# Kernel tuning notes

Hardware: AMD Instinct MI355X
Metric: run time of the kernel (lower is better)

The kernel has to match this reference:

```python
import jax, jax.numpy as jnp
import numpy as np

B, S, SR, SN = 8, 1024, 256, 1024
D1 = 768; D2 = 512; D3 = 768; MVH = 256
H = 12; HDC = 32; HDR = 32; HD = 64
MLP_DIM = 3072
LN_EPS = 1e-6

def _ln(x, w):
    mu = jnp.mean(x, axis=-1, keepdims=True)
    var = jnp.var(x, axis=-1, keepdims=True)
    return (x - mu) * jax.lax.rsqrt(var + LN_EPS) * w

def _rope(x, freqs):
    # x: [B,H,S,dr]; freqs: [S, dr//2] (learned RoPE param)
    emb = jnp.concatenate([freqs, freqs], axis=-1)
    cos = jnp.cos(emb); sin = jnp.sin(emb)
    d = x.shape[-1] // 2
    rot = jnp.concatenate([-x[..., d:], x[..., :d]], axis=-1)
    return x * cos + rot * sin

def _rope_freqs(seq, dim, theta=10.0):
    inv_freq = 1.0 / theta ** (np.arange(0, dim, 2, dtype=np.float32) / dim)
    t = np.arange(seq, dtype=np.float32)
    return jnp.asarray(np.outer(t, inv_freq))

def setup_inputs():
    key = jax.random.key(0)
    ks = iter(jax.random.split(key, 48))
    n = lambda shape, s=0.02: jax.random.normal(next(ks), shape, jnp.float32) * s
    return dict(
        input_q=jax.random.normal(next(ks), (B, S, D1), jnp.float32),
        ln_q_w=jnp.ones((D1,), jnp.float32), ln_kv_w=jnp.ones((D1,), jnp.float32),
        Wt_mq=n((SR, S)), Wt_vq=n((SR, S)), Wt_mkv=n((SR, S)), Wt_vkv=n((SR, S)),
        mq_w1=n((D2, D1)), mq_w2=n((MVH, D2)),
        vq_w1=n((D2, D1)), vq_w2=n((MVH, D2)),
        mkv_w1=n((D2, D1)), mkv_w2=n((MVH, D2)),
        vkv_w1=n((D2, D1)), vkv_w2=n((MVH, D2)),
        dirty_zq=n((1, SR, MVH), 1.0), dirty_zkv=n((1, SR, MVH), 1.0),
        e2de=jnp.array([1.0], jnp.float32),
        Wt_qzu=n((SN, SR)), Wt_kzu=n((SN, SR)), Wt_vzu=n((SN, SR)),
        Wt_qr=n((SN, SR)), Wt_kr=n((SN, S)),
        qz_up=n((D2, MVH)), kz_up=n((D2, MVH)), vz_up=n((D2, MVH)),
        q_w=n((H * HDC, D2)), k_w=n((H * HDC, D2)), v_w=n((D3, D2)),
        qr_w=n((H * HDR, MVH)), kr_w=n((H * HDR, D1)),
        rope_q_freqs=_rope_freqs(SN, HDR), rope_k_freqs=_rope_freqs(SN, HDR),
        out_w=n((D3, D3)), ln2_w=jnp.ones((D3,), jnp.float32),
        mlp_w1=n((MLP_DIM, D3)), mlp_w2=n((D3, MLP_DIM)),
        eps_zq=jax.random.normal(next(ks), (B, SR, MVH), jnp.float32),
        eps_zkv=jax.random.normal(next(ks), (B, SR, MVH), jnp.float32),
    )

def reference(input_q, ln_q_w, ln_kv_w, Wt_mq, Wt_vq, Wt_mkv, Wt_vkv, mq_w1, mq_w2, vq_w1, vq_w2, mkv_w1, mkv_w2, vkv_w1, vkv_w2, dirty_zq, dirty_zkv, e2de, Wt_qzu, Wt_kzu, Wt_vzu, Wt_qr, Wt_kr, qz_up, kz_up, vz_up, q_w, k_w, v_w, qr_w, kr_w, rope_q_freqs, rope_k_freqs, out_w, ln2_w, mlp_w1, mlp_w2, eps_zq, eps_zkv):
    lin = lambda x, w: x @ w.T                       # torch Linear: W is [out, in]
    tlin = lambda x, w: jnp.einsum('bsd,rs->brd', x, w)  # Linear along seq axis
    xq = _ln(input_q, ln_q_w)
    xkv = _ln(input_q, ln_kv_w)  # input_kv = input_q (self-attention)
    # latent VAE mean/var: seq compress S->SR then feature D1->D2->MVH
    mean_zq = lin(lin(tlin(xq, Wt_mq), mq_w1), mq_w2)
    var_zq = lin(lin(tlin(xq, Wt_vq), vq_w1), vq_w2)
    mean_zkv = lin(lin(tlin(xkv, Wt_mkv), mkv_w1), mkv_w2)
    var_zkv = lin(lin(tlin(xkv, Wt_vkv), vkv_w1), vkv_w2)
    zq = mean_zq + (e2de * eps_zq + (1.0 - e2de) * dirty_zq) * jnp.exp(0.5 * var_zq)
    zkv = mean_zkv + (e2de * eps_zkv + (1.0 - e2de) * dirty_zkv) * jnp.exp(0.5 * var_zkv)
    # upsample seq SR->SN and features MVH->D2
    qz = lin(tlin(zq, Wt_qzu), qz_up)
    kz = lin(tlin(zkv, Wt_kzu), kz_up)
    vz = lin(tlin(zkv, Wt_vzu), vz_up)
    qr = lin(tlin(zq, Wt_qr), qr_w)        # [B,SN,H*HDR]
    kr = lin(tlin(input_q, Wt_kr), kr_w)   # [B,SN,H*HDR]
    qz = lin(qz, q_w); kz = lin(kz, k_w); vz = lin(vz, v_w)
    heads = lambda t, d: t.reshape(B, SN, H, d).transpose(0, 2, 1, 3)
    q = jnp.concatenate([heads(qz, HDC), _rope(heads(qr, HDR), rope_q_freqs)], axis=-1)
    k = jnp.concatenate([heads(kz, HDC), _rope(heads(kr, HDR), rope_k_freqs)], axis=-1)
    v = heads(vz, HD)
    scores = jnp.einsum('bhqd,bhkd->bhqk', q, k) / jnp.sqrt(jnp.float32(HD))
    o = jnp.einsum('bhqk,bhkd->bhqd', jax.nn.softmax(scores, axis=-1), v)
    o = o.transpose(0, 2, 1, 3).reshape(B, SN, D3)
    x = lin(o, out_w) + input_q
    y = _ln(x, ln2_w)
    y = lin(jax.nn.gelu(lin(y, mlp_w1), approximate=False), mlp_w2)
    return x + y
```

## Files before the change

kernel.cpp:

```cpp
#include <hip/hip_runtime.h>
#include <math.h>

#define B_   8
#define S_   1024
#define SR_  256
#define SN_  1024
#define D1_  768
#define D2_  512
#define D3_  768
#define MVH_ 256
#define H_   12
#define HD_  64
#define MLP_ 3072

typedef __attribute__((ext_vector_type(8))) short bf16x8;
typedef __attribute__((ext_vector_type(4))) float f32x4;

__device__ inline ushort f2bf(float f) {
  uint u = __float_as_uint(f);
  uint r = (u + 0x7fffu + ((u >> 16) & 1u)) >> 16;
  return (ushort)r;
}
__device__ inline float b2f(ushort u) { return __uint_as_float(((uint)u) << 16); }

__device__ inline void gload16(const void* g, void* l) {
  __builtin_amdgcn_global_load_lds(
      (const __attribute__((address_space(1))) void*)g,
      (__attribute__((address_space(3))) void*)l, 16, 0, 0);
}

__global__ __launch_bounds__(256) void ln_dual(const float* __restrict__ x,
    const float* __restrict__ w1, const float* __restrict__ w2,
    float* __restrict__ o1, float* __restrict__ o2, int D) {
  int row = blockIdx.x;
  const float* xr = x + (size_t)row * D;
  int tid = threadIdx.x;
  float s = 0.f, ss = 0.f;
  for (int i = tid; i < D; i += 256) { float v = xr[i]; s += v; ss += v * v; }
  __shared__ float rs[256];
  __shared__ float rq[256];
  rs[tid] = s; rq[tid] = ss;
  __syncthreads();
  for (int off = 128; off > 0; off >>= 1) {
    if (tid < off) { rs[tid] += rs[tid + off]; rq[tid] += rq[tid + off]; }
    __syncthreads();
  }
  float mu  = rs[0] / (float)D;
  float var = rq[0] / (float)D - mu * mu;
  float inv = rsqrtf(var + 1e-6f);
  for (int i = tid; i < D; i += 256) {
    float v = (xr[i] - mu) * inv;
    o1[(size_t)row * D + i] = v * w1[i];
    if (o2) o2[(size_t)row * D + i] = v * w2[i];
  }
}

__global__ __launch_bounds__(256) void ln_b(const float* __restrict__ x,
    const float* __restrict__ w, ushort* __restrict__ o, int D) {
  int row = blockIdx.x;
  const float* xr = x + (size_t)row * D;
  int tid = threadIdx.x;
  float s = 0.f, ss = 0.f;
  for (int i = tid; i < D; i += 256) { float v = xr[i]; s += v; ss += v * v; }
  __shared__ float rs[256];
  __shared__ float rq[256];
  rs[tid] = s; rq[tid] = ss;
  __syncthreads();
  for (int off = 128; off > 0; off >>= 1) {
    if (tid < off) { rs[tid] += rs[tid + off]; rq[tid] += rq[tid + off]; }
    __syncthreads();
  }
  float mu  = rs[0] / (float)D;
  float var = rq[0] / (float)D - mu * mu;
  float inv = rsqrtf(var + 1e-6f);
  for (int i = tid; i < D; i += 256) {
    float v = (xr[i] - mu) * inv;
    o[(size_t)row * D + i] = f2bf(v * w[i]);
  }
}

__global__ __launch_bounds__(256) void trans_f2b(const float* __restrict__ in,
    ushort* __restrict__ out, int R, int C, long strideEl) {
  __shared__ float tile[32][33];
  int bb = blockIdx.z;
  const float* ib = in + (size_t)bb * strideEl;
  ushort* ob = out + (size_t)bb * strideEl;
  int c0 = blockIdx.x << 5, r0 = blockIdx.y << 5;
  int tx = threadIdx.x & 31, ty = threadIdx.x >> 5;
#pragma unroll
  for (int i = 0; i < 4; ++i)
    tile[ty + 8 * i][tx] = ib[(size_t)(r0 + ty + 8 * i) * C + c0 + tx];
  __syncthreads();
#pragma unroll
  for (int i = 0; i < 4; ++i)
    ob[(size_t)(c0 + ty + 8 * i) * R + r0 + tx] = f2bf(tile[tx][ty + 8 * i]);
}

__global__ __launch_bounds__(256) void trans_b2b(const ushort* __restrict__ in,
    ushort* __restrict__ out, int R, int C, long strideEl) {
  __shared__ ushort tile[32][33];
  int bb = blockIdx.z;
  const ushort* ib = in + (size_t)bb * strideEl;
  ushort* ob = out + (size_t)bb * strideEl;
  int c0 = blockIdx.x << 5, r0 = blockIdx.y << 5;
  int tx = threadIdx.x & 31, ty = threadIdx.x >> 5;
#pragma unroll
  for (int i = 0; i < 4; ++i)
    tile[ty + 8 * i][tx] = ib[(size_t)(r0 + ty + 8 * i) * C + c0 + tx];
  __syncthreads();
#pragma unroll
  for (int i = 0; i < 4; ++i)
    ob[(size_t)(c0 + ty + 8 * i) * R + r0 + tx] = tile[tx][ty + 8 * i];
}

struct ConvTab {
  const float* src[28];
  int off[28];
  int cum[29];
};
__global__ __launch_bounds__(256) void multi_f2b(ConvTab t, ushort* __restrict__ wb,
                                                 int total4) {
  int i = blockIdx.x * 256 + threadIdx.x;
  if (i >= total4) return;
  int ti = 0;
  while (t.cum[ti + 1] <= i) ++ti;
  int j = i - t.cum[ti];
  float4 v = ((const float4*)t.src[ti])[j];
  ushort4 o;
  o.x = f2bf(v.x); o.y = f2bf(v.y); o.z = f2bf(v.z); o.w = f2bf(v.w);
  ((ushort4*)(wb + t.off[ti]))[j] = o;
}

template <int EPI>
__global__ __launch_bounds__(256) void gemm_bf16(const ushort* __restrict__ A, long sA,
    const ushort* __restrict__ Bm, long sB, const float* __restrict__ R,
    void* __restrict__ Cout, long sC, int M, int N, int K) {
  int bb = blockIdx.z;
  const ushort* Ab = A + (size_t)bb * sA;
  const ushort* Bb = Bm + (size_t)bb * sB;
  __shared__ ushort As[128 * 32];
  __shared__ ushort Bs[128 * 32];
  int tid = threadIdx.x;
  int lane = tid & 63, wid = tid >> 6;
  int m0 = blockIdx.y << 7, n0 = blockIdx.x << 7;
  int wm = (wid >> 1) << 6, wn = (wid & 1) << 6;
  f32x4 acc[4][4];
#pragma unroll
  for (int i = 0; i < 4; ++i)
#pragma unroll
    for (int j = 0; j < 4; ++j) acc[i][j] = (f32x4){0.f, 0.f, 0.f, 0.f};
  char* asb = (char*)As;
  char* bsb = (char*)Bs;
  int srow = lane >> 2;
  int skb  = (lane & 3) << 4;
  for (int k0 = 0; k0 < K; k0 += 32) {
    __syncthreads();
#pragma unroll
    for (int i = 0; i < 2; ++i) {
      int rr = wid * 32 + i * 16;
      gload16((const char*)Ab + ((size_t)(m0 + rr + srow) * K + k0) * 2 + skb,
              asb + rr * 64);
      gload16((const char*)Bb + ((size_t)(n0 + rr + srow) * K + k0) * 2 + skb,
              bsb + rr * 64);
    }
    __syncthreads();
    bf16x8 af[4], bf[4];
#pragma unroll
    for (int m = 0; m < 4; ++m)
      af[m] = *(bf16x8*)&As[(wm + m * 16 + (lane & 15)) * 32 + ((lane >> 4) << 3)];
#pragma unroll
    for (int n = 0; n < 4; ++n)
      bf[n] = *(bf16x8*)&Bs[(wn + n * 16 + (lane & 15)) * 32 + ((lane >> 4) << 3)];
#pragma unroll
    for (int m = 0; m < 4; ++m)
#pragma unroll
      for (int n = 0; n < 4; ++n)
        acc[m][n] = __builtin_amdgcn_mfma_f32_16x16x32_bf16(af[m], bf[n], acc[m][n], 0, 0, 0);
  }
  int cr = (lane >> 4) << 2, cc = lane & 15;
#pragma unroll
  for (int m = 0; m < 4; ++m)
#pragma unroll
    for (int n = 0; n < 4; ++n) {
#pragma unroll
      for (int r = 0; r < 4; ++r) {
        int row = m0 + wm + m * 16 + cr + r;
        int col = n0 + wn + n * 16 + cc;
        float v = acc[m][n][r];
        if (EPI == 0) {
          ((ushort*)Cout)[(size_t)bb * sC + (size_t)row * N + col] = f2bf(v);
        } else if (EPI == 1) {
          ((float*)Cout)[(size_t)row * N + col] = v + R[(size_t)row * N + col];
        } else {
          float y = 0.7978845608f * (v + 0.044715f * v * v * v);
          float sg = 1.0f / (1.0f + __expf(-2.0f * y));
          ((ushort*)Cout)[(size_t)row * N + col] = f2bf(v * sg);
        }
      }
    }
}

struct GrpTab {
  const ushort* A[32];
  const ushort* Bm[32];
  ushort* C[32];
};
__global__ __launch_bounds__(256) void gemm_grp(GrpTab t, int M, int N, int K) {
  int zz = blockIdx.z;
  const ushort* Ab = t.A[zz];
  const ushort* Bb = t.Bm[zz];
  ushort* Cb = t.C[zz];
  __shared__ ushort As[128 * 32];
  __shared__ ushort Bs[128 * 32];
  int tid = threadIdx.x;
  int lane = tid & 63, wid = tid >> 6;
  int m0 = blockIdx.y << 7, n0 = blockIdx.x << 7;
  int wm = (wid >> 1) << 6, wn = (wid & 1) << 6;
  f32x4 acc[4][4];
#pragma unroll
  for (int i = 0; i < 4; ++i)
#pragma unroll
    for (int j = 0; j < 4; ++j) acc[i][j] = (f32x4){0.f, 0.f, 0.f, 0.f};
  char* asb = (char*)As;
  char* bsb = (char*)Bs;
  int srow = lane >> 2;
  int skb  = (lane & 3) << 4;
  for (int k0 = 0; k0 < K; k0 += 32) {
    __syncthreads();
#pragma unroll
    for (int i = 0; i < 2; ++i) {
      int rr = wid * 32 + i * 16;
      gload16((const char*)Ab + ((size_t)(m0 + rr + srow) * K + k0) * 2 + skb,
              asb + rr * 64);
      gload16((const char*)Bb + ((size_t)(n0 + rr + srow) * K + k0) * 2 + skb,
              bsb + rr * 64);
    }
    __syncthreads();
    bf16x8 af[4], bf[4];
#pragma unroll
    for (int m = 0; m < 4; ++m)
      af[m] = *(bf16x8*)&As[(wm + m * 16 + (lane & 15)) * 32 + ((lane >> 4) << 3)];
#pragma unroll
    for (int n = 0; n < 4; ++n)
      bf[n] = *(bf16x8*)&Bs[(wn + n * 16 + (lane & 15)) * 32 + ((lane >> 4) << 3)];
#pragma unroll
    for (int m = 0; m < 4; ++m)
#pragma unroll
      for (int n = 0; n < 4; ++n)
        acc[m][n] = __builtin_amdgcn_mfma_f32_16x16x32_bf16(af[m], bf[n], acc[m][n], 0, 0, 0);
  }
  int cr = (lane >> 4) << 2, cc = lane & 15;
#pragma unroll
  for (int m = 0; m < 4; ++m)
#pragma unroll
    for (int n = 0; n < 4; ++n) {
#pragma unroll
      for (int r = 0; r < 4; ++r) {
        int row = m0 + wm + m * 16 + cr + r;
        int col = n0 + wn + n * 16 + cc;
        Cb[(size_t)row * N + col] = f2bf(acc[m][n][r]);
      }
    }
}

__global__ __launch_bounds__(256) void z_combine_b(const ushort* __restrict__ mean,
    const ushort* __restrict__ var, const float* __restrict__ eps,
    const float* __restrict__ dirty, const float* __restrict__ e2de_p,
    ushort* __restrict__ zout, int total, int perBatch) {
  int i = blockIdx.x * 256 + threadIdx.x;
  if (i >= total) return;
  float e = e2de_p[0];
  float v = b2f(mean[i]) +
            (e * eps[i] + (1.0f - e) * dirty[i % perBatch]) * expf(0.5f * b2f(var[i]));
  zout[i] = f2bf(v);
}

__global__ __launch_bounds__(256) void pack_qk_b(const ushort* __restrict__ zf,
    const ushort* __restrict__ rf, const float* __restrict__ freqs,
    ushort* __restrict__ out, float scale) {
  int i = blockIdx.x * 256 + threadIdx.x;
  int d = i & 63;
  int s = (i >> 6) & (S_ - 1);
  int bh = i >> 16;
  int b = bh / H_, h = bh % H_;
  float v;
  if (d < 32) {
    v = b2f(zf[((size_t)(b * S_ + s)) * (H_ * 32) + h * 32 + d]);
  } else {
    int dr = d - 32;
    const ushort* xr = rf + ((size_t)(b * S_ + s)) * (H_ * 32) + h * 32;
    float f = freqs[s * 16 + (dr & 15)];
    float c = cosf(f), sn = sinf(f);
    if (dr < 16) v = b2f(xr[dr]) * c - b2f(xr[dr + 16]) * sn;
    else         v = b2f(xr[dr]) * c + b2f(xr[dr - 16]) * sn;
  }
  out[i] = f2bf(v * scale);
}

__global__ __launch_bounds__(256) void pack_v_b(const ushort* __restrict__ vzf,
    ushort* __restrict__ out) {
  int i = blockIdx.x * 256 + threadIdx.x;
  int d = i & 63;
  int s = (i >> 6) & (S_ - 1);
  int bh = i >> 16;
  int b = bh / H_, h = bh % H_;
  out[i] = vzf[((size_t)(b * S_ + s)) * D3_ + h * 64 + d];
}

__global__ __launch_bounds__(256) void attn_mfma(const ushort* __restrict__ Q,
    const ushort* __restrict__ K, const ushort* __restrict__ V,
    ushort* __restrict__ O) {
  __shared__ ushort lds[16384];
  char* qc = (char*)lds;
  char* kc = (char*)lds + 8192;
  char* vc = (char*)lds + 16384;
  char* pc = (char*)lds + 24576;
  int tid = threadIdx.x, lane = tid & 63, wid = tid >> 6;
  int bh = blockIdx.y, q0 = blockIdx.x << 6;
  int b = bh / H_, h = bh % H_;
  const ushort* Qb = Q + ((size_t)bh * S_ + q0) * HD_;
  const ushort* Kb = K + (size_t)bh * S_ * HD_;
  const ushort* Vb = V + (size_t)bh * S_ * HD_;
  {
    int r = tid >> 2, c0 = (tid & 3) * 32;
    const char* src = (const char*)Qb + r * 128;
    uint4 v0 = *(const uint4*)(src + c0);
    uint4 v1 = *(const uint4*)(src + c0 + 16);
    int sw = (r & 7) << 4;
    *(uint4*)(qc + r * 128 + (c0 ^ sw)) = v0;
    *(uint4*)(qc + r * 128 + ((c0 + 16) ^ sw)) = v1;
  }
  __syncthreads();
  bf16x8 aq[2];
  {
    int r = wid * 16 + (lane & 15);
    int sw = (r & 7) << 4;
#pragma unroll
    for (int kk = 0; kk < 2; ++kk) {
      int c2 = kk * 64 + ((lane >> 4) << 4);
      aq[kk] = *(bf16x8*)(qc + r * 128 + (c2 ^ sw));
    }
  }
  f32x4 o_[4];
  float m_[4], l_[4];
#pragma unroll
  for (int i = 0; i < 4; ++i) { o_[i] = (f32x4){0.f,0.f,0.f,0.f}; m_[i] = -1e30f; l_[i] = 0.f; }

  for (int kt = 0; kt < S_ / 64; ++kt) {
    __syncthreads();
    {
      int r = tid >> 2, c0 = (tid & 3) * 32;
      const char* src = (const char*)(Kb + (size_t)(kt * 64 + r) * HD_);
      uint4 v0 = *(const uint4*)(src + c0);
      uint4 v1 = *(const uint4*)(src + c0 + 16);
      int sw = (r & 7) << 4;
      *(uint4*)(kc + r * 128 + (c0 ^ sw)) = v0;
      *(uint4*)(kc + r * 128 + ((c0 + 16) ^ sw)) = v1;
    }
    {
      int kp = tid & 31, g = tid >> 5, d0 = g * 8;
      const ushort* s0 = Vb + (size_t)(kt * 64 + 2 * kp) * HD_ + d0;
      bf16x8 va = *(const bf16x8*)s0;
      bf16x8 vb2 = *(const bf16x8*)(s0 + HD_);
#pragma unroll
      for (int j = 0; j < 8; ++j) {
        int d = d0 + j;
        uint val = (uint)(ushort)va[j] | ((uint)(ushort)vb2[j] << 16);
        *(uint*)(vc + d * 128 + ((kp * 4) ^ ((d & 7) << 4))) = val;
      }
    }
    __syncthreads();
    f32x4 sacc[4];
#pragma unroll
    for (int ksub = 0; ksub < 4; ++ksub) {
      sacc[ksub] = (f32x4){0.f,0.f,0.f,0.f};
#pragma unroll
      for (int kk = 0; kk < 2; ++kk) {
        int r = ksub * 16 + (lane & 15);
        int c2 = kk * 64 + ((lane >> 4) << 4);
        bf16x8 bk = *(bf16x8*)(kc + r * 128 + (c2 ^ ((r & 7) << 4)));
        sacc[ksub] = __builtin_amdgcn_mfma_f32_16x16x32_bf16(aq[kk], bk, sacc[ksub], 0, 0, 0);
      }
    }
    float p[4][4];
#pragma unroll
    for (int rr = 0; rr < 4; ++rr) {
      float cm = fmaxf(fmaxf(sacc[0][rr], sacc[1][rr]), fmaxf(sacc[2][rr], sacc[3][rr]));
      cm = fmaxf(cm, __shfl_xor(cm, 1));
      cm = fmaxf(cm, __shfl_xor(cm, 2));
      cm = fmaxf(cm, __shfl_xor(cm, 4));
      cm = fmaxf(cm, __shfl_xor(cm, 8));
      float mn = fmaxf(m_[rr], cm);
      float al = __expf(m_[rr] - mn);
      float ps = 0.f;
#pragma unroll
      for (int ksub = 0; ksub < 4; ++ksub) {
        float pv = __expf(sacc[ksub][rr] - mn);
        p[ksub][rr] = pv;
        ps += pv;
      }
      ps += __shfl_xor(ps, 1);
      ps += __shfl_xor(ps, 2);
      ps += __shfl_xor(ps, 4);
      ps += __shfl_xor(ps, 8);
      l_[rr] = l_[rr] * al + ps;
      m_[rr] = mn;
#pragma unroll
      for (int ds = 0; ds < 4; ++ds) o_[ds][rr] *= al;
    }
#pragma unroll
    for (int ksub = 0; ksub < 4; ++ksub)
#pragma unroll
      for (int rr = 0; rr < 4; ++rr) {
        int r = wid * 16 + ((lane >> 4) << 2) + rr;
        int cb = (ksub * 16 + (lane & 15)) * 2;
        *(ushort*)(pc + r * 128 + (cb ^ ((r & 7) << 4))) = f2bf(p[ksub][rr]);
      }
#pragma unroll
    for (int kk2 = 0; kk2 < 2; ++kk2) {
      int rA = wid * 16 + (lane & 15);
      int c2 = kk2 * 64 + ((lane >> 4) << 4);
      bf16x8 ap = *(bf16x8*)(pc + rA * 128 + (c2 ^ ((rA & 7) << 4)));
#pragma unroll
      for (int ds = 0; ds < 4; ++ds) {
        int rB = ds * 16 + (lane & 15);
        bf16x8 bv = *(bf16x8*)(vc + rB * 128 + (c2 ^ ((rB & 7) << 4)));
        o_[ds] = __builtin_amdgcn_mfma_f32_16x16x32_bf16(ap, bv, o_[ds], 0, 0, 0);
      }
    }
  }
#pragma unroll
  for (int rr = 0; rr < 4; ++rr) {
    float inv = 1.f / l_[rr];
    int q = q0 + wid * 16 + ((lane >> 4) << 2) + rr;
#pragma unroll
    for (int ds = 0; ds < 4; ++ds) {
      int d = ds * 16 + (lane & 15);
      O[((size_t)(b * S_ + q)) * D3_ + h * HD_ + d] = f2bf(o_[ds][rr] * inv);
    }
  }
}

extern "C" void kernel_launch(void* const* d_in, const int* in_sizes, int n_in,
                              void* d_out, int out_size, void* d_ws, size_t ws_size,
                              hipStream_t stream) {
  const float* input_q = (const float*)d_in[0];
  const float* ln_q_w  = (const float*)d_in[1];
  const float* ln_kv_w = (const float*)d_in[2];
  const float* dirty_zq  = (const float*)d_in[15];
  const float* dirty_zkv = (const float*)d_in[16];
  const float* e2de    = (const float*)d_in[17];
  const float* rope_q_f = (const float*)d_in[31];
  const float* rope_k_f = (const float*)d_in[32];
  const float* ln2_w   = (const float*)d_in[34];
  const float* eps_zq  = (const float*)d_in[37];
  const float* eps_zkv = (const float*)d_in[38];

  ushort* wsu = (ushort*)d_ws;
  ushort* wb   = wsu;
  float*  xq   = (float*)(wsu + 12124160);
  float*  xkv  = (float*)(wsu + 24707072);
  ushort* xqT  = wsu + 37289984;
  ushort* xkvT = wsu + 43581440;
  ushort* inT  = wsu + 49872896;
  ushort* t1q  = wsu + 12124160;
  ushort* t1kv = wsu + 15269888;
  ushort* t2b  = wsu + 18415616;
  ushort* mv   = wsu + 20512768;
  ushort* zqb  = wsu + 21561344;
  ushort* zkvb = wsu + 22085632;
  ushort* zqT  = wsu + 22609920;
  ushort* zkvT = wsu + 23134208;
  ushort* up   = wsu + 23658496;
  ushort* mid  = wsu + 56164352;
  ushort* tkr  = wsu + 37289984;
  ushort* qzf  = wsu + 68747264;
  ushort* kzf  = wsu + 71892992;
  ushort* qrf  = wsu + 75038720;
  ushort* krf  = wsu + 78184448;
  ushort* vzf  = wsu + 23658496;
  ushort* qp   = wsu + 12124160;
  ushort* kp   = wsu + 43581440;
  ushort* vp   = wsu + 49872896;
  ushort* ofb  = wsu + 56164352;
  float*  xb   = (float*)(wsu + 12124160);
  ushort* ylb  = wsu + 37289984;
  ushort* hm   = wsu + 43581440;

  t2b = wsu + 24707072;
  mv  = wsu + 28901376;
  zqb  = wsu + 30998528;
  zkvb = wsu + 31522816;
  zqT  = wsu + 32047104;
  zkvT = wsu + 32571392;
  up   = wsu + 12124160;
  vzf  = wsu + 20512768;
  qp   = wsu + 33095680;
  qp   = wsu + 12124160;

  const int W_mq = 0,       W_vq = 262144,  W_mkv = 524288, W_vkv = 786432;
  const int Wq1 = 1048576,  Wv1 = 1441792,  Wk1 = 1835008,  Wkv1 = 2228224;
  const int Wq2 = 2621440,  Wv2 = 2752512,  Wk2 = 2883584,  Wkv2 = 3014656;
  const int W_qzu = 3145728, W_kzu = 3407872, W_vzu = 3670016, W_qr = 3932160;
  const int W_kr = 4194304, W_qzup = 5242880, W_kzup = 5373952, W_vzup = 5505024;
  const int W_qw = 5636096, W_kw = 5832704,  W_vw = 6029312,  W_qrw = 6422528;
  const int W_krw = 6520832, W_ow = 6815744, W_m1 = 7405568,  W_m2 = 9764864;
  (void)W_vq; (void)W_vkv;

  ln_dual<<<B_ * S_, 256, 0, stream>>>(input_q, ln_q_w, ln_kv_w, xq, xkv, D1_);

  {
    dim3 g(D1_ / 32, S_ / 32, B_);
    trans_f2b<<<g, 256, 0, stream>>>(xq, xqT, S_, D1_, (long)S_ * D1_);
    trans_f2b<<<g, 256, 0, stream>>>(xkv, xkvT, S_, D1_, (long)S_ * D1_);
    trans_f2b<<<g, 256, 0, stream>>>(input_q, inT, S_, D1_, (long)S_ * D1_);
  }

  {
    ConvTab t;
    const int srcIdx[28] = {3,4,5,6, 7,9,11,13, 8,10,12,14, 18,19,20,21, 22,
                            23,24,25, 26,27, 28, 29, 30, 33, 35, 36};
    const int sz[28] = {262144,262144,262144,262144, 393216,393216,393216,393216,
                        131072,131072,131072,131072, 262144,262144,262144,262144,
                        1048576, 131072,131072,131072, 196608,196608, 393216,
                        98304, 294912, 589824, 2359296, 2359296};
    int off = 0, c4 = 0;
    for (int i = 0; i < 28; ++i) {
      t.src[i] = (const float*)d_in[srcIdx[i]];
      t.off[i] = off;
      t.cum[i] = c4;
      off += sz[i];
      c4 += sz[i] / 4;
    }
    t.cum[28] = c4;
    multi_f2b<<<(c4 + 255) / 256, 256, 0, stream>>>(t, wb, c4);
  }

  long sXT = (long)S_ * D1_;

  {
    GrpTab t;
    for (int c = 0; c < 2; ++c)
      for (int b = 0; b < 8; ++b) {
        int z = c * 8 + b;
        t.A[z] = wb + (c == 0 ? W_mq : W_mkv);
        t.Bm[z] = (c == 0 ? xqT : xkvT) + (size_t)b * sXT;
        t.C[z] = (c == 0 ? t1q : t1kv) + (size_t)b * 512 * 768;
      }
    dim3 g(D1_ / 128, 512 / 128, 16);
    gemm_grp<<<g, 256, 0, stream>>>(t, 512, D1_, S_);
  }
  {
    GrpTab t;
    const int wo[4] = {Wq1, Wv1, Wk1, Wkv1};
    for (int c = 0; c < 4; ++c)
      for (int b = 0; b < 8; ++b) {
        int z = c * 8 + b;
        ushort* t1 = (c < 2 ? t1q : t1kv);
        t.A[z] = t1 + (size_t)b * 512 * 768 + (size_t)(c & 1) * 256 * 768;
        t.Bm[z] = wb + wo[c];
        t.C[z] = t2b + (size_t)z * 256 * 512;
      }
    dim3 g(D2_ / 128, 256 / 128, 32);
    gemm_grp<<<g, 256, 0, stream>>>(t, 256, D2_, D1_);
  }
  {
    GrpTab t;
    const int wo[4] = {Wq2, Wv2, Wk2, Wkv2};
    for (int c = 0; c < 4; ++c)
      for (int b = 0; b < 8; ++b) {
        int z = c * 8 + b;
        t.A[z] = t2b + (size_t)z * 256 * 512;
        t.Bm[z] = wb + wo[c];
        t.C[z] = mv + (size_t)z * 256 * 256;
      }
    dim3 g(MVH_ / 128, 256 / 128, 32);
    gemm_grp<<<g, 256, 0, stream>>>(t, 256, MVH_, D2_);
  }
  z_combine_b<<<(B_ * SR_ * MVH_) / 256, 256, 0, stream>>>(mv, mv + 8 * 65536,
      eps_zq, dirty_zq, e2de, zqb, B_ * SR_ * MVH_, SR_ * MVH_);
  z_combine_b<<<(B_ * SR_ * MVH_) / 256, 256, 0, stream>>>(mv + 16 * 65536,
      mv + 24 * 65536, eps_zkv, dirty_zkv, e2de, zkvb, B_ * SR_ * MVH_, SR_ * MVH_);
  {
    dim3 g(MVH_ / 32, SR_ / 32, B_);
    trans_b2b<<<g, 256, 0, stream>>>(zqb, zqT, SR_, MVH_, (long)SR_ * MVH_);
    trans_b2b<<<g, 256, 0, stream>>>(zkvb, zkvT, SR_, MVH_, (long)SR_ * MVH_);
  }
  {
    GrpTab t;
    const int wo[4] = {W_qzu, W_kzu, W_vzu, W_qr};
    for (int c = 0; c < 4; ++c)
      for (int b = 0; b < 8; ++b) {
        int z = c * 8 + b;
        t.A[z] = wb + wo[c];
        t.Bm[z] = ((c == 0 || c == 3) ? zqT : zkvT) + (size_t)b * 65536;
        t.C[z] = up + (size_t)z * 1024 * 256;
      }
    dim3 g(MVH_ / 128, SN_ / 128, 32);
    gemm_grp<<<g, 256, 0, stream>>>(t, SN_, MVH_, SR_);
  }
  {
    GrpTab t;
    const int wo[3] = {W_qzup, W_kzup, W_vzup};
    for (int c = 0; c < 3; ++c) {
      t.A[c] = up + (size_t)c * 8 * 1024 * 256;
      t.Bm[c] = wb + wo[c];
      t.C[c] = mid + (size_t)c * 8192 * 512;
    }
    dim3 g(D2_ / 128, (B_ * SN_) / 128, 3);
    gemm_grp<<<g, 256, 0, stream>>>(t, B_ * SN_, D2_, MVH_);
  }
  {
    dim3 g(384 / 128, (B_ * SN_) / 128, 1);
    gemm_bf16<0><<<g, 256, 0, stream>>>(up + (size_t)3 * 8 * 1024 * 256, 0,
        wb + W_qrw, 0, nullptr, qrf, 0, B_ * SN_, 384, MVH_);
  }
  {
    GrpTab t;
    t.A[0] = mid;                 t.Bm[0] = wb + W_qw; t.C[0] = qzf;
    t.A[1] = mid + (size_t)8192 * 512; t.Bm[1] = wb + W_kw; t.C[1] = kzf;
    dim3 g(384 / 128, (B_ * SN_) / 128, 2);
    gemm_grp<<<g, 256, 0, stream>>>(t, B_ * SN_, 384, D2_);
  }
  {
    dim3 g(D3_ / 128, (B_ * SN_) / 128, 1);
    gemm_bf16<0><<<g, 256, 0, stream>>>(mid + (size_t)2 * 8192 * 512, 0,
        wb + W_vw, 0, nullptr, vzf, 0, B_ * SN_, D3_, D2_);
  }
  {
    dim3 g(D1_ / 128, SN_ / 128, B_);
    gemm_bf16<0><<<g, 256, 0, stream>>>(wb + W_kr, 0, inT, sXT, nullptr, tkr,
        (long)SN_ * D1_, SN_, D1_, S_);
  }
  {
    dim3 g(384 / 128, (B_ * SN_) / 128, 1);
    gemm_bf16<0><<<g, 256, 0, stream>>>(tkr, 0, wb + W_krw, 0, nullptr, krf, 0,
        B_ * SN_, 384, D1_);
  }

  int tot = B_ * H_ * S_ * HD_;
  pack_qk_b<<<tot / 256, 256, 0, stream>>>(qzf, qrf, rope_q_f, qp, 0.125f);
  pack_qk_b<<<tot / 256, 256, 0, stream>>>(kzf, krf, rope_k_f, kp, 1.0f);
  pack_v_b<<<tot / 256, 256, 0, stream>>>(vzf, vp);

  {
    dim3 g(S_ / 64, B_ * H_);
    attn_mfma<<<g, 256, 0, stream>>>(qp, kp, vp, ofb);
  }

  {
    dim3 g(D3_ / 128, (B_ * SN_) / 128);
    gemm_bf16<1><<<g, 256, 0, stream>>>(ofb, 0, wb + W_ow, 0, input_q, xb, 0,
                                        B_ * SN_, D3_, D3_);
  }
  ln_b<<<B_ * SN_, 256, 0, stream>>>(xb, ln2_w, ylb, D3_);
  {
    dim3 g(MLP_ / 128, (B_ * SN_) / 128);
    gemm_bf16<2><<<g, 256, 0, stream>>>(ylb, 0, wb + W_m1, 0, nullptr, hm, 0,
                                        B_ * SN_, MLP_, D3_);
  }
  {
    dim3 g(D3_ / 128, (B_ * SN_) / 128);
    gemm_bf16<1><<<g, 256, 0, stream>>>(hm, 0, wb + W_m2, 0, xb, (float*)d_out, 0,
                                        B_ * SN_, D3_, MLP_);
  }
}
```

Before: 589.4 us.

## Add XCD-aware block swizzle, bf16 LN outputs, vectorized packing and RoPE tables

Remaps workgroup indices in the GEMM and attention kernels so that neighbouring tiles land on the same XCD, which should improve L2 reuse. LayerNorm now writes bf16 directly and the following transposes read bf16, halving that traffic. The pack kernels are vectorized to 8 elements per thread and read precomputed cos/sin tables instead of evaluating trig per element. The swizzle adds index arithmetic, and trans_b2b must exist in the hidden code.

```diff
diff --git a/kernel.cpp b/kernel.cpp
--- a/kernel.cpp
+++ b/kernel.cpp
@@ -29,9 +29,15 @@
       (__attribute__((address_space(3))) void*)l, 16, 0, 0);
 }
 
-__global__ __launch_bounds__(256) void ln_dual(const float* __restrict__ x,
+__device__ inline int xcd_swz(int lin, int n) {
+  int xcd = lin & 7, idx = lin >> 3;
+  int q = n >> 3, r = n & 7;
+  return (xcd < r ? xcd * (q + 1) : r * (q + 1) + (xcd - r) * q) + idx;
+}
+
+__global__ __launch_bounds__(256) void ln_dual_b(const float* __restrict__ x,
     const float* __restrict__ w1, const float* __restrict__ w2,
-    float* __restrict__ o1, float* __restrict__ o2, int D) {
+    ushort* __restrict__ o1, ushort* __restrict__ o2, int D) {
   int row = blockIdx.x;
   const float* xr = x + (size_t)row * D;
   int tid = threadIdx.x;
@@ -50,8 +56,8 @@
   float inv = rsqrtf(var + 1e-6f);
   for (int i = tid; i < D; i += 256) {
     float v = (xr[i] - mu) * inv;
-    o1[(size_t)row * D + i] = v * w1[i];
-    if (o2) o2[(size_t)row * D + i] = v * w2[i];
+    o1[(size_t)row * D + i] = f2bf(v * w1[i]);
+    o2[(size_t)row * D + i] = f2bf(v * w2[i]);
   }
 }
 
@@ -131,18 +137,32 @@
   ((ushort4*)(wb + t.off[ti]))[j] = o;
 }
 
+__global__ __launch_bounds__(256) void rope_tab(const float* __restrict__ fq,
+    const float* __restrict__ fk, float* __restrict__ ctq, float* __restrict__ stq,
+    float* __restrict__ ctk, float* __restrict__ stk, int n) {
+  int i = blockIdx.x * 256 + threadIdx.x;
+  if (i >= n) return;
+  float a = fq[i]; ctq[i] = cosf(a); stq[i] = sinf(a);
+  float c = fk[i]; ctk[i] = cosf(c); stk[i] = sinf(c);
+}
+
 template <int EPI>
 __global__ __launch_bounds__(256) void gemm_bf16(const ushort* __restrict__ A, long sA,
     const ushort* __restrict__ Bm, long sB, const float* __restrict__ R,
     void* __restrict__ Cout, long sC, int M, int N, int K) {
-  int bb = blockIdx.z;
+  int gx = gridDim.x, gy = gridDim.y;
+  int nwg = gx * gy * gridDim.z;
+  int lin = ((int)blockIdx.z * gy + (int)blockIdx.y) * gx + (int)blockIdx.x;
+  lin = xcd_swz(lin, nwg);
+  int bx = lin % gx, tt = lin / gx;
+  int by = tt % gy, bb = tt / gy;
   const ushort* Ab = A + (size_t)bb * sA;
   const ushort* Bb = Bm + (size_t)bb * sB;
   __shared__ ushort As[128 * 32];
   __shared__ ushort Bs[128 * 32];
   int tid = threadIdx.x;
   int lane = tid & 63, wid = tid >> 6;
-  int m0 = blockIdx.y << 7, n0 = blockIdx.x << 7;
+  int m0 = by << 7, n0 = bx << 7;
   int wm = (wid >> 1) << 6, wn = (wid & 1) << 6;
   f32x4 acc[4][4];
 #pragma unroll
@@ -206,7 +226,12 @@
   ushort* C[32];
 };
 __global__ __launch_bounds__(256) void gemm_grp(GrpTab t, int M, int N, int K) {
-  int zz = blockIdx.z;
+  int gx = gridDim.x, gy = gridDim.y;
+  int nwg = gx * gy * gridDim.z;
+  int lin = ((int)blockIdx.z * gy + (int)blockIdx.y) * gx + (int)blockIdx.x;
+  lin = xcd_swz(lin, nwg);
+  int bx = lin % gx, tt = lin / gx;
+  int by = tt % gy, zz = tt / gy;
   const ushort* Ab = t.A[zz];
   const ushort* Bb = t.Bm[zz];
   ushort* Cb = t.C[zz];
@@ -214,7 +239,7 @@
   __shared__ ushort Bs[128 * 32];
   int tid = threadIdx.x;
   int lane = tid & 63, wid = tid >> 6;
-  int m0 = blockIdx.y << 7, n0 = blockIdx.x << 7;
+  int m0 = by << 7, n0 = bx << 7;
   int wm = (wid >> 1) << 6, wn = (wid & 1) << 6;
   f32x4 acc[4][4];
 #pragma unroll
@@ -275,36 +300,54 @@
   zout[i] = f2bf(v);
 }
 
-__global__ __launch_bounds__(256) void pack_qk_b(const ushort* __restrict__ zf,
-    const ushort* __restrict__ rf, const float* __restrict__ freqs,
-    ushort* __restrict__ out, float scale) {
-  int i = blockIdx.x * 256 + threadIdx.x;
-  int d = i & 63;
+__global__ __launch_bounds__(256) void pack_qk_b8(const ushort* __restrict__ zf,
+    const ushort* __restrict__ rf, const float* __restrict__ ct,
+    const float* __restrict__ st, ushort* __restrict__ out, float scale) {
+  int i8 = blockIdx.x * 256 + threadIdx.x;
+  int i = i8 << 3;
+  int d0 = i & 63;
   int s = (i >> 6) & (S_ - 1);
   int bh = i >> 16;
   int b = bh / H_, h = bh % H_;
-  float v;
-  if (d < 32) {
-    v = b2f(zf[((size_t)(b * S_ + s)) * (H_ * 32) + h * 32 + d]);
+  short res[8];
+  if (d0 < 32) {
+    bf16x8 v = *(const bf16x8*)(zf + ((size_t)(b * S_ + s)) * (H_ * 32) + h * 32 + d0);
+#pragma unroll
+    for (int j = 0; j < 8; ++j) res[j] = (short)f2bf(b2f((ushort)v[j]) * scale);
   } else {
-    int dr = d - 32;
     const ushort* xr = rf + ((size_t)(b * S_ + s)) * (H_ * 32) + h * 32;
-    float f = freqs[s * 16 + (dr & 15)];
-    float c = cosf(f), sn = sinf(f);
-    if (dr < 16) v = b2f(xr[dr]) * c - b2f(xr[dr + 16]) * sn;
-    else         v = b2f(xr[dr]) * c + b2f(xr[dr - 16]) * sn;
-  }
-  out[i] = f2bf(v * scale);
-}
-
-__global__ __launch_bounds__(256) void pack_v_b(const ushort* __restrict__ vzf,
+    int dr0 = d0 - 32;
+    if (dr0 < 16) {
+      bf16x8 xa = *(const bf16x8*)(xr + dr0);
+      bf16x8 xb2 = *(const bf16x8*)(xr + dr0 + 16);
+#pragma unroll
+      for (int j = 0; j < 8; ++j) {
+        float c = ct[s * 16 + dr0 + j], sn = st[s * 16 + dr0 + j];
+        res[j] = (short)f2bf((b2f((ushort)xa[j]) * c - b2f((ushort)xb2[j]) * sn) * scale);
+      }
+    } else {
+      bf16x8 xa = *(const bf16x8*)(xr + dr0);
+      bf16x8 xb2 = *(const bf16x8*)(xr + dr0 - 16);
+#pragma unroll
+      for (int j = 0; j < 8; ++j) {
+        float c = ct[s * 16 + dr0 - 16 + j], sn = st[s * 16 + dr0 - 16 + j];
+        res[j] = (short)f2bf((b2f((ushort)xa[j]) * c + b2f((ushort)xb2[j]) * sn) * scale);
+      }
+    }
+  }
+  *(bf16x8*)(out + i) = *(bf16x8*)res;
+}
+
+__global__ __launch_bounds__(256) void pack_v_b8(const ushort* __restrict__ vzf,
     ushort* __restrict__ out) {
-  int i = blockIdx.x * 256 + threadIdx.x;
-  int d = i & 63;
+  int i8 = blockIdx.x * 256 + threadIdx.x;
+  int i = i8 << 3;
+  int d0 = i & 63;
   int s = (i >> 6) & (S_ - 1);
   int bh = i >> 16;
   int b = bh / H_, h = bh % H_;
-  out[i] = vzf[((size_t)(b * S_ + s)) * D3_ + h * 64 + d];
+  bf16x8 v = *(const bf16x8*)(vzf + ((size_t)(b * S_ + s)) * D3_ + h * 64 + d0);
+  *(bf16x8*)(out + i) = v;
 }
 
 __global__ __launch_bounds__(256) void attn_mfma(const ushort* __restrict__ Q,
@@ -316,7 +359,12 @@
   char* vc = (char*)lds + 16384;
   char* pc = (char*)lds + 24576;
   int tid = threadIdx.x, lane = tid & 63, wid = tid >> 6;
-  int bh = blockIdx.y, q0 = blockIdx.x << 6;
+  int nwg = gridDim.x * gridDim.y;
+  int lin = (int)blockIdx.y * gridDim.x + (int)blockIdx.x;
+  lin = xcd_swz(lin, nwg);
+  int qt = lin % gridDim.x;
+  int bh = lin / gridDim.x;
+  int q0 = qt << 6;
   int b = bh / H_, h = bh % H_;
   const ushort* Qb = Q + ((size_t)bh * S_ + q0) * HD_;
   const ushort* Kb = K + (size_t)bh * S_ * HD_;
@@ -457,62 +505,54 @@
   const float* eps_zkv = (const float*)d_in[38];
 
   ushort* wsu = (ushort*)d_ws;
-  ushort* wb   = wsu;
-  float*  xq   = (float*)(wsu + 12124160);
-  float*  xkv  = (float*)(wsu + 24707072);
-  ushort* xqT  = wsu + 37289984;
-  ushort* xkvT = wsu + 43581440;
-  ushort* inT  = wsu + 49872896;
-  ushort* t1q  = wsu + 12124160;
-  ushort* t1kv = wsu + 15269888;
-  ushort* t2b  = wsu + 18415616;
-  ushort* mv   = wsu + 20512768;
-  ushort* zqb  = wsu + 21561344;
-  ushort* zkvb = wsu + 22085632;
-  ushort* zqT  = wsu + 22609920;
-  ushort* zkvT = wsu + 23134208;
-  ushort* up   = wsu + 23658496;
-  ushort* mid  = wsu + 56164352;
-  ushort* tkr  = wsu + 37289984;
-  ushort* qzf  = wsu + 68747264;
-  ushort* kzf  = wsu + 71892992;
-  ushort* qrf  = wsu + 75038720;
-  ushort* krf  = wsu + 78184448;
-  ushort* vzf  = wsu + 23658496;
-  ushort* qp   = wsu + 12124160;
-  ushort* kp   = wsu + 43581440;
-  ushort* vp   = wsu + 49872896;
-  ushort* ofb  = wsu + 56164352;
-  float*  xb   = (float*)(wsu + 12124160);
-  ushort* ylb  = wsu + 37289984;
-  ushort* hm   = wsu + 43581440;
-
-  t2b = wsu + 24707072;
-  mv  = wsu + 28901376;
-  zqb  = wsu + 30998528;
-  zkvb = wsu + 31522816;
-  zqT  = wsu + 32047104;
-  zkvT = wsu + 32571392;
-  up   = wsu + 12124160;
-  vzf  = wsu + 20512768;
-  qp   = wsu + 33095680;
-  qp   = wsu + 12124160;
-
-  const int W_mq = 0,       W_vq = 262144,  W_mkv = 524288, W_vkv = 786432;
+  ushort* wb    = wsu;
+  ushort* xq_b  = wsu + 12124160;
+  ushort* xkv_b = wsu + 18415616;
+  ushort* xqT   = wsu + 37289984;
+  ushort* xkvT  = wsu + 43581440;
+  ushort* inT   = wsu + 49872896;
+  ushort* t1q   = wsu + 12124160;
+  ushort* t1kv  = wsu + 15269888;
+  ushort* t2b   = wsu + 24707072;
+  ushort* mv    = wsu + 28901376;
+  ushort* zqb   = wsu + 30998528;
+  ushort* zkvb  = wsu + 31522816;
+  ushort* zqT   = wsu + 32047104;
+  ushort* zkvT  = wsu + 32571392;
+  ushort* up    = wsu + 12124160;
+  ushort* vzf   = wsu + 20512768;
+  ushort* mid   = wsu + 56164352;
+  ushort* tkr   = wsu + 37289984;
+  ushort* qzf   = wsu + 68747264;
+  ushort* kzf   = wsu + 71892992;
+  ushort* qrf   = wsu + 75038720;
+  ushort* krf   = wsu + 78184448;
+  float*  ctq   = (float*)(wsu + 81330176);
+  float*  stq   = ctq + 16384;
+  float*  ctk   = ctq + 32768;
+  float*  stk   = ctq + 49152;
+  ushort* qp    = wsu + 12124160;
+  ushort* kp    = wsu + 43581440;
+  ushort* vp    = wsu + 49872896;
+  ushort* ofb   = wsu + 56164352;
+  float*  xb    = (float*)(wsu + 12124160);
+  ushort* ylb   = wsu + 37289984;
+  ushort* hm    = wsu + 43581440;
+
+  const int W_mq = 0,       W_mkv = 524288;
   const int Wq1 = 1048576,  Wv1 = 1441792,  Wk1 = 1835008,  Wkv1 = 2228224;
   const int Wq2 = 2621440,  Wv2 = 2752512,  Wk2 = 2883584,  Wkv2 = 3014656;
   const int W_qzu = 3145728, W_kzu = 3407872, W_vzu = 3670016, W_qr = 3932160;
   const int W_kr = 4194304, W_qzup = 5242880, W_kzup = 5373952, W_vzup = 5505024;
   const int W_qw = 5636096, W_kw = 5832704,  W_vw = 6029312,  W_qrw = 6422528;
   const int W_krw = 6520832, W_ow = 6815744, W_m1 = 7405568,  W_m2 = 9764864;
-  (void)W_vq; (void)W_vkv;
-
-  ln_dual<<<B_ * S_, 256, 0, stream>>>(input_q, ln_q_w, ln_kv_w, xq, xkv, D1_);
+
+  ln_dual_b<<<B_ * S_, 256, 0, stream>>>(input_q, ln_q_w, ln_kv_w, xq_b, xkv_b, D1_);
 
   {
     dim3 g(D1_ / 32, S_ / 32, B_);
-    trans_f2b<<<g, 256, 0, stream>>>(xq, xqT, S_, D1_, (long)S_ * D1_);
-    trans_f2b<<<g, 256, 0, stream>>>(xkv, xkvT, S_, D1_, (long)S_ * D1_);
+    trans_b2b<<<g, 256, 0, stream>>>(xq_b, xqT, S_, D1_, (long)S_ * D1_);
+    trans_b2b<<<g, 256, 0, stream>>>(xkv_b, xkvT, S_, D1_, (long)S_ * D1_);
     trans_f2b<<<g, 256, 0, stream>>>(input_q, inT, S_, D1_, (long)S_ * D1_);
   }
 
@@ -534,6 +574,7 @@
     }
     t.cum[28] = c4;
     multi_f2b<<<(c4 + 255) / 256, 256, 0, stream>>>(t, wb, c4);
+    rope_tab<<<64, 256, 0, stream>>>(rope_q_f, rope_k_f, ctq, stq, ctk, stk, 16384);
   }
 
   long sXT = (long)S_ * D1_;
@@ -617,7 +658,7 @@
   }
   {
     GrpTab t;
-    t.A[0] = mid;                 t.Bm[0] = wb + W_qw; t.C[0] = qzf;
+    t.A[0] = mid;                      t.Bm[0] = wb + W_qw; t.C[0] = qzf;
     t.A[1] = mid + (size_t)8192 * 512; t.Bm[1] = wb + W_kw; t.C[1] = kzf;
     dim3 g(384 / 128, (B_ * SN_) / 128, 2);
     gemm_grp<<<g, 256, 0, stream>>>(t, B_ * SN_, 384, D2_);
@@ -638,10 +679,10 @@
         B_ * SN_, 384, D1_);
   }
 
-  int tot = B_ * H_ * S_ * HD_;
-  pack_qk_b<<<tot / 256, 256, 0, stream>>>(qzf, qrf, rope_q_f, qp, 0.125f);
-  pack_qk_b<<<tot / 256, 256, 0, stream>>>(kzf, krf, rope_k_f, kp, 1.0f);
-  pack_v_b<<<tot / 256, 256, 0, stream>>>(vzf, vp);
+  int chunks = (B_ * H_ * S_ * HD_) / 8;
+  pack_qk_b8<<<chunks / 256, 256, 0, stream>>>(qzf, qrf, ctq, stq, qp, 0.125f);
+  pack_qk_b8<<<chunks / 256, 256, 0, stream>>>(kzf, krf, ctk, stk, kp, 1.0f);
+  pack_v_b8<<<chunks / 256, 256, 0, stream>>>(vzf, vp);
 
   {
     dim3 g(S_ / 64, B_ * H_);
```

Measured after the change: 542.9 us. 7.9% less time.
